# Performance work log

Measured on AMD Instinct MI355X. Metric: run time of the kernel, lower is better.

The kernel has to match this reference:

```python
import jax, jax.numpy as jnp
import numpy as np

D_FEATURE = 512
D_K = 512
B, LQ, N = 64, 128, 2048
NEG_BIAS = 1e10


def setup_inputs() -> dict:
    key = jax.random.key(0)
    k1, k2, k3, k4, k5, k6 = jax.random.split(key, 6)
    # xavier_uniform bound for Linear(d_feature -> d_k), weight shape [d_k, d_feature]
    bound = float(np.sqrt(6.0 / (D_FEATURE + D_K)))
    metal_feature = jax.random.normal(k1, (B, LQ, D_FEATURE), dtype=jnp.float32)
    x = jax.random.normal(k2, (B, N, D_FEATURE), dtype=jnp.float32)
    mask = jax.random.randint(k3, (B, N), 0, 2, dtype=jnp.int32)
    W_q = jax.random.uniform(k4, (D_K, D_FEATURE), jnp.float32, -bound, bound)
    W_k = jax.random.uniform(k5, (D_K, D_FEATURE), jnp.float32, -bound, bound)
    W_v = jax.random.uniform(k6, (D_K, D_FEATURE), jnp.float32, -bound, bound)
    return {"metal_feature": metal_feature, "x": x, "mask": mask,
            "W_q": W_q, "W_k": W_k, "W_v": W_v}


def reference(metal_feature, x, mask, W_q, W_k, W_v):
    # Q: [B, Lq, d_k], K/V: [B, N, d_k]  (torch Linear: y = x @ W.T, no bias)
    Q = jnp.einsum('blf,kf->blk', metal_feature, W_q)
    K = jnp.einsum('bnf,kf->bnk', x, W_k)
    V = jnp.einsum('bnf,kf->bnk', x, W_v)
    scale = 1.0 / jnp.sqrt(jnp.float32(D_K))
    # scores: [B, Lq, N] with additive mask bias (mask broadcast over queries)
    scores = jnp.einsum('blk,bnk->bln', Q, K) * scale
    scores = scores - (1.0 - mask[:, None, :].astype(scores.dtype)) * NEG_BIAS
    attn = jax.nn.softmax(scores, axis=-1)
    out = jnp.einsum('bln,bnk->blk', attn, V)
    # relu; squeeze(1) is a no-op for Lq>1; dropout identity at eval
    return jax.nn.relu(out)
```

## Files before the change

### kernel.cpp

```cpp
#include <hip/hip_runtime.h>

typedef __attribute__((ext_vector_type(4))) float   f32x4;
typedef __attribute__((ext_vector_type(8))) __bf16  bf16x8;
typedef unsigned short u16;
typedef __attribute__((ext_vector_type(8))) unsigned short u16x8;
typedef __attribute__((ext_vector_type(4))) unsigned short u16x4;

__device__ __forceinline__ u16 f2bf(float f) {
  unsigned u = __builtin_bit_cast(unsigned, f);
  u += 0x7fffu + ((u >> 16) & 1u);
  return (u16)(u >> 16);
}
__device__ __forceinline__ float bf2f(u16 h) {
  unsigned u = ((unsigned)h) << 16;
  return __builtin_bit_cast(float, u);
}
__device__ __forceinline__ void gld16(const void* g, void* l) {
  __builtin_amdgcn_global_load_lds(
      (const __attribute__((address_space(1))) void*)g,
      (__attribute__((address_space(3))) void*)l, 16, 0, 0);
}


#define SB __builtin_amdgcn_sched_barrier(0)
#define SYNC_MID do { SB; __builtin_amdgcn_s_barrier(); \
  asm volatile("s_waitcnt lgkmcnt(0)" ::: "memory"); SB; } while(0)
#define SYNC_END do { SB; __builtin_amdgcn_s_barrier(); SB; } while(0)
#define VM4 do { SB; asm volatile("s_waitcnt vmcnt(4)" ::: "memory"); SB; } while(0)
#define VM0 do { SB; asm volatile("s_waitcnt vmcnt(0)" ::: "memory"); SB; } while(0)

#define LDA(AQ, S, I0) \
  _Pragma("unroll") for (int f = 0; f < 2; ++f) \
  _Pragma("unroll") for (int s = 0; s < 2; ++s) { \
    const int rl = ((I0)+f)*16 + lr; \
    AQ[f*2+s] = *(const u16x8*)&SM[((S)*2 + wr)*8192 + rl*64 + (((s*4+lc) ^ (rl&7))*8)]; }

#define LDB(S) \
  _Pragma("unroll") for (int j = 0; j < 4; ++j) \
  _Pragma("unroll") for (int s = 0; s < 2; ++s) { \
    const int rl = (wc&1)*64 + j*16 + lr; \
    bq[j][s] = *(const u16x8*)&SM[32768 + ((S)*2 + (wc>>1))*8192 + rl*64 + (((s*4+lc) ^ (rl&7))*8)]; }

#define MM(AQ, I0) do { __builtin_amdgcn_s_setprio(1); \
  _Pragma("unroll") for (int f = 0; f < 2; ++f) \
  _Pragma("unroll") for (int j = 0; j < 4; ++j) \
  _Pragma("unroll") for (int s = 0; s < 2; ++s) \
    acc[(I0)+f][j] = __builtin_amdgcn_mfma_f32_16x16x32_bf16( \
      __builtin_bit_cast(bf16x8, AQ[f*2+s]), __builtin_bit_cast(bf16x8, bq[j][s]), \
      acc[(I0)+f][j], 0, 0, 0); \
  __builtin_amdgcn_s_setprio(0); } while(0)

__global__ __launch_bounds__(512, 1)
void kv8_k(const u16* __restrict__ xb, const u16* __restrict__ Wkv,
           u16* __restrict__ Kc, u16* __restrict__ Vt)
{
  __shared__ u16 SM[65536];
  const int t = threadIdx.x;
  const int w = t >> 6, lane = t & 63;
  const int wr = w >> 2, wc = w & 3;
  const int lr = lane & 15, lc = lane >> 4;

  int bx, by;
  if (gridDim.y == 64) {
    const int h = (int)(blockIdx.y * 4 + blockIdx.x);
    const int c = h & 7, i = h >> 3;
    by = c + 8 * (i & 7);
    bx = i >> 3;
  } else { bx = blockIdx.x; by = blockIdx.y; }
  const int n0 = bx * 256;
  const u16* xg = xb + (long)by * 2048 * 512;

  f32x4 acc[8][4];
#pragma unroll
  for (int i = 0; i < 8; i++)
#pragma unroll
    for (int j = 0; j < 4; j++) acc[i][j] = f32x4{0.f, 0.f, 0.f, 0.f};
  u16x8 bq[4][2];

  auto stageA = [&](int TT, int h) {
#pragma unroll
    for (int r = 0; r < 2; ++r) {
      const int c = r * 512 + t;
      const int row = c >> 3, slot = c & 7;
      const u16* g = xg + (long)((TT >> 3) * 256 + h * 128 + row) * 512
                        + (TT & 7) * 64 + ((slot ^ (row & 7)) * 8);
      gld16(g, (void*)&SM[((TT & 1) * 2 + h) * 8192 + c * 8]);
    }
  };
  auto stageB = [&](int TT, int h) {
#pragma unroll
    for (int r = 0; r < 2; ++r) {
      const int c = r * 512 + t;
      const int row = c >> 3, slot = c & 7;
      const u16* g = Wkv + (long)(n0 + h * 128 + row) * 512
                         + (TT & 7) * 64 + ((slot ^ (row & 7)) * 8);
      gld16(g, (void*)&SM[32768 + ((TT & 1) * 2 + h) * 8192 + c * 8]);
    }
  };
  auto epi = [&](int mt) {
#pragma unroll
    for (int i = 0; i < 8; i++)
#pragma unroll
      for (int j = 0; j < 4; j++) {
        const int ml = mt * 256 + wr * 128 + i * 16 + lc * 4;
        const int n  = n0 + wc * 64 + j * 16 + lr;
        if (n0 < 512) {
#pragma unroll
          for (int ii = 0; ii < 4; ii++)
            Kc[((long)by * 2048 + ml + ii) * 512 + n] = f2bf(acc[i][j][ii]);
        } else {
          u16x4 hh;
#pragma unroll
          for (int ii = 0; ii < 4; ii++) hh[ii] = f2bf(acc[i][j][ii]);
          *(u16x4*)(Vt + ((long)by * 512 + (n - 512)) * 2048 + ml) = hh;
        }
        acc[i][j] = f32x4{0.f, 0.f, 0.f, 0.f};
      }
  };

  stageA(0, 0); stageA(0, 1);
  stageB(0, 0); stageB(0, 1);
  stageB(1, 0); stageB(1, 1);
  VM4;
  __builtin_amdgcn_s_barrier(); SB;

  const int NT = 64;
#pragma unroll 1
  for (int I = 0; I < NT / 2; ++I) {
    const int a = 2 * I, b = 2 * I + 1;
    const bool g2 = (a + 2) < NT;
    const bool g3 = (b + 2) < NT;
    { u16x8 aq[4]; LDB(0); LDA(aq, 0, 0); stageA(b, 0);
      SYNC_MID; MM(aq, 0); SYNC_END; }
    { u16x8 aq[4]; LDA(aq, 0, 2); stageA(b, 1);
      SYNC_MID; MM(aq, 2); SYNC_END; }
    { u16x8 aq[4]; LDA(aq, 0, 4); if (g2) stageB(a + 2, 0);
      SYNC_MID; MM(aq, 4); SYNC_END; }
    { u16x8 aq[4]; LDA(aq, 0, 6); if (g2) stageB(a + 2, 1);
      SYNC_MID; MM(aq, 6); if (g2) { VM4; } else { VM0; } SYNC_END; }
    { u16x8 aq[4]; LDB(1); LDA(aq, 1, 0); if (g2) stageA(a + 2, 0);
      SYNC_MID; MM(aq, 0); SYNC_END; }
    { u16x8 aq[4]; LDA(aq, 1, 2); if (g2) stageA(a + 2, 1);
      SYNC_MID; MM(aq, 2); SYNC_END; }
    { u16x8 aq[4]; LDA(aq, 1, 4); if (g3) stageB(b + 2, 0);
      SYNC_MID; MM(aq, 4); SYNC_END; }
    { u16x8 aq[4]; LDA(aq, 1, 6); if (g3) stageB(b + 2, 1);
      SYNC_MID; MM(aq, 6); if (g3) { VM4; } else { VM0; } SYNC_END; }
    if ((I & 3) == 3) epi(I >> 2);
  }
}

template<int EPI>
__global__ __launch_bounds__(256)
void gemm_k(const u16* __restrict__ Ap, const u16* __restrict__ Bp,
            void* __restrict__ Cp, const int* __restrict__ maskp,
            int K, long sA, long sB, long sC, long sM, int ldc, float scale)
{
  __shared__ u16 Asb[2][4096];
  __shared__ u16 Bs [2][4096];

  const int t = threadIdx.x, z = blockIdx.z;
  const int n0 = blockIdx.x * 128, m0 = blockIdx.y * 128;
  const int KT = K / 32;
  const u16* Ab = Ap + (long)z * sA;
  const u16* Bb = Bp + (long)z * sB;

  const int w = t >> 6, lane = t & 63;
  const int m0w = (w >> 1) * 64, n0w = (w & 1) * 64;
  const int lr = lane & 15, lc = lane >> 4;

  f32x4 acc[4][4];
#pragma unroll
  for (int i = 0; i < 4; i++)
#pragma unroll
    for (int j = 0; j < 4; j++) acc[i][j] = f32x4{0.f, 0.f, 0.f, 0.f};

  auto stage = [&](int buf, int kt) {
#pragma unroll
    for (int i = 0; i < 2; i++) {
      int chunk = w * 2 + i, row = chunk * 16 + (lane >> 2), cc = lane & 3;
      const u16* g = Ab + (long)(m0 + row) * K + kt * 32 + ((cc ^ ((row >> 1) & 3)) << 3);
      gld16(g, (void*)&Asb[buf][chunk * 512]);
    }
#pragma unroll
    for (int i = 0; i < 2; i++) {
      int chunk = w * 2 + i, row = chunk * 16 + (lane >> 2), cc = lane & 3;
      const u16* g = Bb + (long)(n0 + row) * K + kt * 32 + ((cc ^ ((row >> 1) & 3)) << 3);
      gld16(g, (void*)&Bs[buf][chunk * 512]);
    }
  };
  auto compute = [&](int buf) {
    bf16x8 af[4], bv[4];
#pragma unroll
    for (int f = 0; f < 4; f++) {
      const int R = m0w + f * 16 + lr;
      af[f] = __builtin_bit_cast(bf16x8,
          *(const u16x8*)&Asb[buf][R * 32 + ((lc ^ ((R >> 1) & 3)) << 3)]);
      const int R2 = n0w + f * 16 + lr;
      bv[f] = __builtin_bit_cast(bf16x8,
          *(const u16x8*)&Bs[buf][R2 * 32 + ((lc ^ ((R2 >> 1) & 3)) << 3)]);
    }
#pragma unroll
    for (int i = 0; i < 4; i++)
#pragma unroll
      for (int j = 0; j < 4; j++)
        acc[i][j] = __builtin_amdgcn_mfma_f32_16x16x32_bf16(af[i], bv[j], acc[i][j], 0, 0, 0);
  };

  stage(0, 0);
  __syncthreads();
  int cur = 0;
  for (int kt = 1; kt < KT; ++kt) {
    stage(cur ^ 1, kt);
    compute(cur);
    __syncthreads();
    cur ^= 1;
  }
  compute(cur);

#pragma unroll
  for (int i = 0; i < 4; i++) {
#pragma unroll
    for (int j = 0; j < 4; j++) {
      const int mb = m0 + m0w + i * 16 + lc * 4;
      const int n  = n0 + n0w + j * 16 + lr;
      if constexpr (EPI == 0) {
        u16* C = (u16*)Cp + (long)z * sC;
#pragma unroll
        for (int ii = 0; ii < 4; ii++)
          C[(long)(mb + ii) * ldc + n] = f2bf(acc[i][j][ii]);
      } else if constexpr (EPI == 2) {
        const int* mk = maskp + (long)z * sM;
        u16* C = (u16*)Cp + (long)z * sC;
        const float bias = mk[n] ? 0.f : -1e10f;
#pragma unroll
        for (int ii = 0; ii < 4; ii++)
          C[(long)(mb + ii) * ldc + n] = f2bf(acc[i][j][ii] * scale + bias);
      } else {
        float* C = (float*)Cp + (long)z * sC;
#pragma unroll
        for (int ii = 0; ii < 4; ii++)
          C[(long)(mb + ii) * ldc + n] = fmaxf(acc[i][j][ii], 0.f);
      }
    }
  }
}

__global__ __launch_bounds__(256)
void wconv_k(const float* __restrict__ Wq, const float* __restrict__ Wk,
             const float* __restrict__ Wv, u16* __restrict__ Wb)
{
  long i4 = (long)blockIdx.x * 256 + threadIdx.x;
  long e  = i4 * 4;
  const float* W = (e < 262144) ? Wq : (e < 524288 ? Wk : Wv);
  long off = e & 262143;
  f32x4 f = *(const f32x4*)(W + off);
  u16x4 h;
#pragma unroll
  for (int j = 0; j < 4; j++) h[j] = f2bf(f[j]);
  *(u16x4*)(Wb + e) = h;
}

__global__ __launch_bounds__(256)
void cvt_k(const float* __restrict__ in, u16* __restrict__ out)
{
  long i = ((long)blockIdx.x * 256 + threadIdx.x) * 8;
  f32x4 a = *(const f32x4*)(in + i);
  f32x4 b = *(const f32x4*)(in + i + 4);
  u16x8 h;
#pragma unroll
  for (int j = 0; j < 4; j++) { h[j] = f2bf(a[j]); h[4 + j] = f2bf(b[j]); }
  *(u16x8*)(out + i) = h;
}

__global__ __launch_bounds__(256)
void softmax_k(u16* __restrict__ S)
{
  const long row = blockIdx.x;
  const int  t   = threadIdx.x;
  u16* R = S + row * 2048;
  u16x8 v = *(const u16x8*)(R + t * 8);
  float f[8];
#pragma unroll
  for (int j = 0; j < 8; j++) f[j] = bf2f(v[j]);
  float m = f[0];
#pragma unroll
  for (int j = 1; j < 8; j++) m = fmaxf(m, f[j]);
#pragma unroll
  for (int off = 32; off > 0; off >>= 1) m = fmaxf(m, __shfl_xor(m, off));
  __shared__ float red[4], red2[4];
  const int w = t >> 6;
  if ((t & 63) == 0) red[w] = m;
  __syncthreads();
  m = fmaxf(fmaxf(red[0], red[1]), fmaxf(red[2], red[3]));
  float e[8], s = 0.f;
#pragma unroll
  for (int j = 0; j < 8; j++) { e[j] = __expf(f[j] - m); s += e[j]; }
#pragma unroll
  for (int off = 32; off > 0; off >>= 1) s += __shfl_xor(s, off);
  if ((t & 63) == 0) red2[w] = s;
  __syncthreads();
  s = red2[0] + red2[1] + red2[2] + red2[3];
  const float inv = 1.f / s;
  u16x8 o;
#pragma unroll
  for (int j = 0; j < 8; j++) o[j] = f2bf(e[j] * inv);
  *(u16x8*)(R + t * 8) = o;
}

extern "C" void kernel_launch(void* const* d_in, const int* in_sizes, int n_in,
                              void* d_out, int out_size, void* d_ws, size_t ws_size,
                              hipStream_t stream)
{
  const float* mf   = (const float*)d_in[0];
  const float* x    = (const float*)d_in[1];
  const int*   mask = (const int*)d_in[2];
  const float* Wq   = (const float*)d_in[3];
  const float* Wk   = (const float*)d_in[4];
  const float* Wv   = (const float*)d_in[5];
  float* out = (float*)d_out;

  u16* ws  = (u16*)d_ws;
  u16* Wb  = ws;
  u16* mfb = Wb + 786432;
  u16* Qb  = mfb + 4194304;
  u16* dyn = Qb + 4194304;

  const size_t fixedB = (size_t)(786432 + 4194304 + 4194304) * 2;
  int CB = 64;
  while (CB > 1 && fixedB + (size_t)CB * 6815744ull > ws_size) CB >>= 1;

  u16* xbc = dyn;
  u16* Kc  = xbc + (size_t)CB * 1048576;
  u16* Vtc = Kc  + (size_t)CB * 1048576;
  u16* Sc  = Vtc + (size_t)CB * 1048576;

  const float scale = 0.044194173824159216f;

  wconv_k<<<768, 256, 0, stream>>>(Wq, Wk, Wv, Wb);
  cvt_k<<<2048, 256, 0, stream>>>(mf, mfb);

  gemm_k<0><<<dim3(4, 64, 1), 256, 0, stream>>>(
      mfb, Wb, Qb, nullptr, 512, 0, 0, 0, 0, 512, 1.f);

  for (int bc = 0; bc < 64; bc += CB) {
    const float* xc = x + (long)bc * 2048 * 512;
    cvt_k<<<CB * 512, 256, 0, stream>>>(xc, xbc);
    kv8_k<<<dim3(4, CB, 1), 512, 0, stream>>>(xbc, Wb + 262144, Kc, Vtc);
    gemm_k<2><<<dim3(16, 1, CB), 256, 0, stream>>>(
        Qb + (long)bc * 65536, Kc, Sc, mask + (long)bc * 2048,
        512, 65536, 1048576, 262144, 2048, 2048, scale);
    softmax_k<<<CB * 128, 256, 0, stream>>>(Sc);
    gemm_k<3><<<dim3(4, 1, CB), 256, 0, stream>>>(
        Sc, Vtc, out + (long)bc * 65536, nullptr,
        2048, 262144, 1048576, 65536, 0, 512, 1.f);
  }
}
```

Measured before the change: 392.0 us.

## Fuse fp32-to-bf16 conversion of x into KV GEMM via producer warps

Removes the separate cvt_k pass over x and its bf16 workspace buffer. The KV projection kernel gains 256 producer threads that load fp32 x tiles into registers, convert them to bf16 and write them into shared memory. They stay in lockstep with the 512 MFMA consumer threads through the existing barrier schedule. This saves a full read and write of x in bf16 and one kernel launch, at the cost of more threads and registers per block and a producer path that may not keep pace with the MFMA loop.

```diff
diff --git a/kernel.cpp b/kernel.cpp
--- a/kernel.cpp
+++ b/kernel.cpp
@@ -23,8 +23,8 @@
 
 
 #define SB __builtin_amdgcn_sched_barrier(0)
-#define SYNC_MID do { SB; __builtin_amdgcn_s_barrier(); \
-  asm volatile("s_waitcnt lgkmcnt(0)" ::: "memory"); SB; } while(0)
+#define LK0 asm volatile("s_waitcnt lgkmcnt(0)" ::: "memory")
+#define SYNC_MID do { SB; __builtin_amdgcn_s_barrier(); LK0; SB; } while(0)
 #define SYNC_END do { SB; __builtin_amdgcn_s_barrier(); SB; } while(0)
 #define VM4 do { SB; asm volatile("s_waitcnt vmcnt(4)" ::: "memory"); SB; } while(0)
 #define VM0 do { SB; asm volatile("s_waitcnt vmcnt(0)" ::: "memory"); SB; } while(0)
@@ -50,15 +50,12 @@
       acc[(I0)+f][j], 0, 0, 0); \
   __builtin_amdgcn_s_setprio(0); } while(0)
 
-__global__ __launch_bounds__(512, 1)
-void kv8_k(const u16* __restrict__ xb, const u16* __restrict__ Wkv,
+__global__ __launch_bounds__(768, 3)
+void kv8_k(const float* __restrict__ x, const u16* __restrict__ Wkv,
            u16* __restrict__ Kc, u16* __restrict__ Vt)
 {
   __shared__ u16 SM[65536];
   const int t = threadIdx.x;
-  const int w = t >> 6, lane = t & 63;
-  const int wr = w >> 2, wc = w & 3;
-  const int lr = lane & 15, lc = lane >> 4;
 
   int bx, by;
   if (gridDim.y == 64) {
@@ -68,85 +65,131 @@
     bx = i >> 3;
   } else { bx = blockIdx.x; by = blockIdx.y; }
   const int n0 = bx * 256;
-  const u16* xg = xb + (long)by * 2048 * 512;
-
-  f32x4 acc[8][4];
-#pragma unroll
-  for (int i = 0; i < 8; i++)
-#pragma unroll
-    for (int j = 0; j < 4; j++) acc[i][j] = f32x4{0.f, 0.f, 0.f, 0.f};
-  u16x8 bq[4][2];
-
-  auto stageA = [&](int TT, int h) {
-#pragma unroll
-    for (int r = 0; r < 2; ++r) {
-      const int c = r * 512 + t;
-      const int row = c >> 3, slot = c & 7;
-      const u16* g = xg + (long)((TT >> 3) * 256 + h * 128 + row) * 512
-                        + (TT & 7) * 64 + ((slot ^ (row & 7)) * 8);
-      gld16(g, (void*)&SM[((TT & 1) * 2 + h) * 8192 + c * 8]);
-    }
-  };
-  auto stageB = [&](int TT, int h) {
-#pragma unroll
-    for (int r = 0; r < 2; ++r) {
-      const int c = r * 512 + t;
-      const int row = c >> 3, slot = c & 7;
-      const u16* g = Wkv + (long)(n0 + h * 128 + row) * 512
-                         + (TT & 7) * 64 + ((slot ^ (row & 7)) * 8);
-      gld16(g, (void*)&SM[32768 + ((TT & 1) * 2 + h) * 8192 + c * 8]);
-    }
-  };
-  auto epi = [&](int mt) {
+  const float* xgf = x + (long)by * 2048 * 512;
+
+  const int NT = 64;
+
+  if (t < 512) {
+    const int w = t >> 6, lane = t & 63;
+    const int wr = w >> 2, wc = w & 3;
+    const int lr = lane & 15, lc = lane >> 4;
+
+    f32x4 acc[8][4];
 #pragma unroll
     for (int i = 0; i < 8; i++)
 #pragma unroll
-      for (int j = 0; j < 4; j++) {
-        const int ml = mt * 256 + wr * 128 + i * 16 + lc * 4;
-        const int n  = n0 + wc * 64 + j * 16 + lr;
-        if (n0 < 512) {
-#pragma unroll
-          for (int ii = 0; ii < 4; ii++)
-            Kc[((long)by * 2048 + ml + ii) * 512 + n] = f2bf(acc[i][j][ii]);
-        } else {
-          u16x4 hh;
-#pragma unroll
-          for (int ii = 0; ii < 4; ii++) hh[ii] = f2bf(acc[i][j][ii]);
-          *(u16x4*)(Vt + ((long)by * 512 + (n - 512)) * 2048 + ml) = hh;
+      for (int j = 0; j < 4; j++) acc[i][j] = f32x4{0.f, 0.f, 0.f, 0.f};
+    u16x8 bq[4][2];
+
+    auto stageB = [&](int TT, int h) {
+#pragma unroll
+      for (int r = 0; r < 2; ++r) {
+        const int c = r * 512 + t;
+        const int row = c >> 3, slot = c & 7;
+        const u16* g = Wkv + (long)(n0 + h * 128 + row) * 512
+                           + (TT & 7) * 64 + ((slot ^ (row & 7)) * 8);
+        gld16(g, (void*)&SM[32768 + ((TT & 1) * 2 + h) * 8192 + c * 8]);
+      }
+    };
+    auto epi = [&](int mt) {
+#pragma unroll
+      for (int i = 0; i < 8; i++)
+#pragma unroll
+        for (int j = 0; j < 4; j++) {
+          const int ml = mt * 256 + wr * 128 + i * 16 + lc * 4;
+          const int n  = n0 + wc * 64 + j * 16 + lr;
+          if (n0 < 512) {
+#pragma unroll
+            for (int ii = 0; ii < 4; ii++)
+              Kc[((long)by * 2048 + ml + ii) * 512 + n] = f2bf(acc[i][j][ii]);
+          } else {
+            u16x4 hh;
+#pragma unroll
+            for (int ii = 0; ii < 4; ii++) hh[ii] = f2bf(acc[i][j][ii]);
+            *(u16x4*)(Vt + ((long)by * 512 + (n - 512)) * 2048 + ml) = hh;
+          }
+          acc[i][j] = f32x4{0.f, 0.f, 0.f, 0.f};
         }
-        acc[i][j] = f32x4{0.f, 0.f, 0.f, 0.f};
+    };
+
+    stageB(0, 0); stageB(0, 1);
+    stageB(1, 0); stageB(1, 1);
+    VM4;
+    __builtin_amdgcn_s_barrier(); SB;
+
+#pragma unroll 1
+    for (int I = 0; I < NT / 2; ++I) {
+      const int a = 2 * I, b = 2 * I + 1;
+      const bool g2 = (a + 2) < NT;
+      const bool g3 = (b + 2) < NT;
+      { u16x8 aq[4]; LDB(0); LDA(aq, 0, 0);
+        SYNC_MID; MM(aq, 0); SYNC_END; }
+      { u16x8 aq[4]; LDA(aq, 0, 2);
+        SYNC_MID; MM(aq, 2); SYNC_END; }
+      { u16x8 aq[4]; LDA(aq, 0, 4); if (g2) stageB(a + 2, 0);
+        SYNC_MID; MM(aq, 4); SYNC_END; }
+      { u16x8 aq[4]; LDA(aq, 0, 6); if (g2) stageB(a + 2, 1);
+        SYNC_MID; MM(aq, 6); if (g2) { VM4; } else { VM0; } SYNC_END; }
+      { u16x8 aq[4]; LDB(1); LDA(aq, 1, 0);
+        SYNC_MID; MM(aq, 0); SYNC_END; }
+      { u16x8 aq[4]; LDA(aq, 1, 2);
+        SYNC_MID; MM(aq, 2); SYNC_END; }
+      { u16x8 aq[4]; LDA(aq, 1, 4); if (g3) stageB(b + 2, 0);
+        SYNC_MID; MM(aq, 4); SYNC_END; }
+      { u16x8 aq[4]; LDA(aq, 1, 6); if (g3) stageB(b + 2, 1);
+        SYNC_MID; MM(aq, 6); if (g3) { VM4; } else { VM0; } SYNC_END; }
+      if ((I & 3) == 3) epi(I >> 2);
+    }
+  } else {
+    const int pt = t - 512;
+
+    f32x4 P0[8], P1[8], P2[8], P3[8];
+
+    auto pissue = [&](f32x4* P, int TT, int h) {
+#pragma unroll
+      for (int r = 0; r < 4; ++r) {
+        const int c = r * 256 + pt;
+        const int row = c >> 3, slot = c & 7;
+        const float* g = xgf + (long)((TT >> 3) * 256 + h * 128 + row) * 512
+                             + (TT & 7) * 64 + ((slot ^ (row & 7)) * 8);
+        P[2 * r]     = *(const f32x4*)g;
+        P[2 * r + 1] = *(const f32x4*)(g + 4);
       }
-  };
-
-  stageA(0, 0); stageA(0, 1);
-  stageB(0, 0); stageB(0, 1);
-  stageB(1, 0); stageB(1, 1);
-  VM4;
-  __builtin_amdgcn_s_barrier(); SB;
-
-  const int NT = 64;
+    };
+    auto pwrite = [&](const f32x4* P, int TT, int h) {
+#pragma unroll
+      for (int r = 0; r < 4; ++r) {
+        const int c = r * 256 + pt;
+        u16x8 o;
+#pragma unroll
+        for (int j = 0; j < 4; ++j) {
+          o[j]     = f2bf(P[2 * r][j]);
+          o[4 + j] = f2bf(P[2 * r + 1][j]);
+        }
+        *(u16x8*)&SM[((TT & 1) * 2 + h) * 8192 + c * 8] = o;
+      }
+    };
+
+    pissue(P2, 0, 0); pissue(P3, 0, 1);
+    pwrite(P2, 0, 0); pwrite(P3, 0, 1);
+    pissue(P0, 1, 0); pissue(P1, 1, 1);
+    LK0; SB;
+    __builtin_amdgcn_s_barrier(); SB;
+
 #pragma unroll 1
-  for (int I = 0; I < NT / 2; ++I) {
-    const int a = 2 * I, b = 2 * I + 1;
-    const bool g2 = (a + 2) < NT;
-    const bool g3 = (b + 2) < NT;
-    { u16x8 aq[4]; LDB(0); LDA(aq, 0, 0); stageA(b, 0);
-      SYNC_MID; MM(aq, 0); SYNC_END; }
-    { u16x8 aq[4]; LDA(aq, 0, 2); stageA(b, 1);
-      SYNC_MID; MM(aq, 2); SYNC_END; }
-    { u16x8 aq[4]; LDA(aq, 0, 4); if (g2) stageB(a + 2, 0);
-      SYNC_MID; MM(aq, 4); SYNC_END; }
-    { u16x8 aq[4]; LDA(aq, 0, 6); if (g2) stageB(a + 2, 1);
-      SYNC_MID; MM(aq, 6); if (g2) { VM4; } else { VM0; } SYNC_END; }
-    { u16x8 aq[4]; LDB(1); LDA(aq, 1, 0); if (g2) stageA(a + 2, 0);
-      SYNC_MID; MM(aq, 0); SYNC_END; }
-    { u16x8 aq[4]; LDA(aq, 1, 2); if (g2) stageA(a + 2, 1);
-      SYNC_MID; MM(aq, 2); SYNC_END; }
-    { u16x8 aq[4]; LDA(aq, 1, 4); if (g3) stageB(b + 2, 0);
-      SYNC_MID; MM(aq, 4); SYNC_END; }
-    { u16x8 aq[4]; LDA(aq, 1, 6); if (g3) stageB(b + 2, 1);
-      SYNC_MID; MM(aq, 6); if (g3) { VM4; } else { VM0; } SYNC_END; }
-    if ((I & 3) == 3) epi(I >> 2);
+    for (int I = 0; I < NT / 2; ++I) {
+      const int a = 2 * I, b = 2 * I + 1;
+      const int aT = (a + 2 < NT) ? a + 2 : NT - 2;
+      const int bT = (b + 2 < NT) ? b + 2 : NT - 1;
+      { pissue(P2, aT, 0); pwrite(P0, b, 0); LK0; SYNC_MID; SYNC_END; }
+      { SYNC_MID; SYNC_END; }
+      { pissue(P3, aT, 1); pwrite(P1, b, 1); LK0; SYNC_MID; SYNC_END; }
+      { SYNC_MID; SYNC_END; }
+      { pissue(P0, bT, 0); pwrite(P2, aT, 0); LK0; SYNC_MID; SYNC_END; }
+      { SYNC_MID; SYNC_END; }
+      { pissue(P1, bT, 1); pwrite(P3, aT, 1); LK0; SYNC_MID; SYNC_END; }
+      { SYNC_MID; SYNC_END; }
+    }
   }
 }
 
@@ -328,11 +371,10 @@
 
   const size_t fixedB = (size_t)(786432 + 4194304 + 4194304) * 2;
   int CB = 64;
-  while (CB > 1 && fixedB + (size_t)CB * 6815744ull > ws_size) CB >>= 1;
-
-  u16* xbc = dyn;
-  u16* Kc  = xbc + (size_t)CB * 1048576;
-  u16* Vtc = Kc  + (size_t)CB * 1048576;
+  while (CB > 1 && fixedB + (size_t)CB * 4718592ull > ws_size) CB >>= 1;
+
+  u16* Kc  = dyn;
+  u16* Vtc = Kc + (size_t)CB * 1048576;
   u16* Sc  = Vtc + (size_t)CB * 1048576;
 
   const float scale = 0.044194173824159216f;
@@ -345,8 +387,7 @@
 
   for (int bc = 0; bc < 64; bc += CB) {
     const float* xc = x + (long)bc * 2048 * 512;
-    cvt_k<<<CB * 512, 256, 0, stream>>>(xc, xbc);
-    kv8_k<<<dim3(4, CB, 1), 512, 0, stream>>>(xbc, Wb + 262144, Kc, Vtc);
+    kv8_k<<<dim3(4, CB, 1), 768, 0, stream>>>(xc, Wb + 262144, Kc, Vtc);
     gemm_k<2><<<dim3(16, 1, CB), 256, 0, stream>>>(
         Qb + (long)bc * 65536, Kc, Sc, mask + (long)bc * 2048,
         512, 65536, 1048576, 262144, 2048, 2048, scale);
```

Result: slower. 812.0 us (+107.1%).

## Fuse x fp32-to-bf16 conversion into KV projection GEMM A-operand loads

Applied to the files above, without the earlier changes.

Drops the separate cvt_k pass over x. The KV GEMM kernel now reads fp32 x straight from global memory into registers and converts it to bf16 there. Only the weight tile stays staged in shared memory, which halves the LDS footprint and the workspace needed per batch chunk. The cost is that A loads are no longer prefetched or shared through LDS. Each wave column and each of the four N-blocks re-reads fp32 x, roughly doubling the bytes read per element, and global load latency is exposed inside each MFMA step.

```diff
diff --git a/kernel.cpp b/kernel.cpp
--- a/kernel.cpp
+++ b/kernel.cpp
@@ -23,23 +23,28 @@
 
 
 #define SB __builtin_amdgcn_sched_barrier(0)
-#define SYNC_MID do { SB; __builtin_amdgcn_s_barrier(); \
-  asm volatile("s_waitcnt lgkmcnt(0)" ::: "memory"); SB; } while(0)
+#define LK0 asm volatile("s_waitcnt lgkmcnt(0)" ::: "memory")
+#define SYNC_MID do { SB; __builtin_amdgcn_s_barrier(); LK0; SB; } while(0)
 #define SYNC_END do { SB; __builtin_amdgcn_s_barrier(); SB; } while(0)
 #define VM4 do { SB; asm volatile("s_waitcnt vmcnt(4)" ::: "memory"); SB; } while(0)
-#define VM0 do { SB; asm volatile("s_waitcnt vmcnt(0)" ::: "memory"); SB; } while(0)
-
-#define LDA(AQ, S, I0) \
+
+#define FLDA(AQ, TT, I0) \
   _Pragma("unroll") for (int f = 0; f < 2; ++f) \
   _Pragma("unroll") for (int s = 0; s < 2; ++s) { \
-    const int rl = ((I0)+f)*16 + lr; \
-    AQ[f*2+s] = *(const u16x8*)&SM[((S)*2 + wr)*8192 + rl*64 + (((s*4+lc) ^ (rl&7))*8)]; }
+    const int rg = (((TT) >> 3) * 256) + wr * 128 + ((I0) + f) * 16 + lr; \
+    const float* g = xgf + (long)rg * 512 + (((TT) & 7) * 64) + ((s * 4 + lc) * 8); \
+    const f32x4 lo = *(const f32x4*)g; \
+    const f32x4 hi = *(const f32x4*)(g + 4); \
+    bf16x8 v; \
+    _Pragma("unroll") for (int j = 0; j < 4; ++j) { \
+      v[j] = (__bf16)lo[j]; v[4 + j] = (__bf16)hi[j]; } \
+    AQ[f*2+s] = __builtin_bit_cast(u16x8, v); }
 
 #define LDB(S) \
   _Pragma("unroll") for (int j = 0; j < 4; ++j) \
   _Pragma("unroll") for (int s = 0; s < 2; ++s) { \
     const int rl = (wc&1)*64 + j*16 + lr; \
-    bq[j][s] = *(const u16x8*)&SM[32768 + ((S)*2 + (wc>>1))*8192 + rl*64 + (((s*4+lc) ^ (rl&7))*8)]; }
+    bq[j][s] = *(const u16x8*)&SM[((S)*2 + (wc>>1))*8192 + rl*64 + (((s*4+lc) ^ (rl&7))*8)]; }
 
 #define MM(AQ, I0) do { __builtin_amdgcn_s_setprio(1); \
   _Pragma("unroll") for (int f = 0; f < 2; ++f) \
@@ -51,10 +56,10 @@
   __builtin_amdgcn_s_setprio(0); } while(0)
 
 __global__ __launch_bounds__(512, 1)
-void kv8_k(const u16* __restrict__ xb, const u16* __restrict__ Wkv,
+void kv8_k(const float* __restrict__ x, const u16* __restrict__ Wkv,
            u16* __restrict__ Kc, u16* __restrict__ Vt)
 {
-  __shared__ u16 SM[65536];
+  __shared__ u16 SM[32768];
   const int t = threadIdx.x;
   const int w = t >> 6, lane = t & 63;
   const int wr = w >> 2, wc = w & 3;
@@ -68,7 +73,7 @@
     bx = i >> 3;
   } else { bx = blockIdx.x; by = blockIdx.y; }
   const int n0 = bx * 256;
-  const u16* xg = xb + (long)by * 2048 * 512;
+  const float* xgf = x + (long)by * 2048 * 512;
 
   f32x4 acc[8][4];
 #pragma unroll
@@ -77,16 +82,6 @@
     for (int j = 0; j < 4; j++) acc[i][j] = f32x4{0.f, 0.f, 0.f, 0.f};
   u16x8 bq[4][2];
 
-  auto stageA = [&](int TT, int h) {
-#pragma unroll
-    for (int r = 0; r < 2; ++r) {
-      const int c = r * 512 + t;
-      const int row = c >> 3, slot = c & 7;
-      const u16* g = xg + (long)((TT >> 3) * 256 + h * 128 + row) * 512
-                        + (TT & 7) * 64 + ((slot ^ (row & 7)) * 8);
-      gld16(g, (void*)&SM[((TT & 1) * 2 + h) * 8192 + c * 8]);
-    }
-  };
   auto stageB = [&](int TT, int h) {
 #pragma unroll
     for (int r = 0; r < 2; ++r) {
@@ -94,7 +89,7 @@
       const int row = c >> 3, slot = c & 7;
       const u16* g = Wkv + (long)(n0 + h * 128 + row) * 512
                          + (TT & 7) * 64 + ((slot ^ (row & 7)) * 8);
-      gld16(g, (void*)&SM[32768 + ((TT & 1) * 2 + h) * 8192 + c * 8]);
+      gld16(g, (void*)&SM[((TT & 1) * 2 + h) * 8192 + c * 8]);
     }
   };
   auto epi = [&](int mt) {
@@ -118,7 +113,6 @@
       }
   };
 
-  stageA(0, 0); stageA(0, 1);
   stageB(0, 0); stageB(0, 1);
   stageB(1, 0); stageB(1, 1);
   VM4;
@@ -130,22 +124,22 @@
     const int a = 2 * I, b = 2 * I + 1;
     const bool g2 = (a + 2) < NT;
     const bool g3 = (b + 2) < NT;
-    { u16x8 aq[4]; LDB(0); LDA(aq, 0, 0); stageA(b, 0);
+    { u16x8 aq[4]; FLDA(aq, a, 0); LDB(0);
       SYNC_MID; MM(aq, 0); SYNC_END; }
-    { u16x8 aq[4]; LDA(aq, 0, 2); stageA(b, 1);
+    { u16x8 aq[4]; FLDA(aq, a, 2);
       SYNC_MID; MM(aq, 2); SYNC_END; }
-    { u16x8 aq[4]; LDA(aq, 0, 4); if (g2) stageB(a + 2, 0);
+    { u16x8 aq[4]; FLDA(aq, a, 4); if (g2) stageB(a + 2, 0);
       SYNC_MID; MM(aq, 4); SYNC_END; }
-    { u16x8 aq[4]; LDA(aq, 0, 6); if (g2) stageB(a + 2, 1);
-      SYNC_MID; MM(aq, 6); if (g2) { VM4; } else { VM0; } SYNC_END; }
-    { u16x8 aq[4]; LDB(1); LDA(aq, 1, 0); if (g2) stageA(a + 2, 0);
+    { u16x8 aq[4]; FLDA(aq, a, 6); if (g2) stageB(a + 2, 1);
+      SYNC_MID; MM(aq, 6); SYNC_END; }
+    { u16x8 aq[4]; FLDA(aq, b, 0); LDB(1);
       SYNC_MID; MM(aq, 0); SYNC_END; }
-    { u16x8 aq[4]; LDA(aq, 1, 2); if (g2) stageA(a + 2, 1);
+    { u16x8 aq[4]; FLDA(aq, b, 2);
       SYNC_MID; MM(aq, 2); SYNC_END; }
-    { u16x8 aq[4]; LDA(aq, 1, 4); if (g3) stageB(b + 2, 0);
+    { u16x8 aq[4]; FLDA(aq, b, 4); if (g3) stageB(b + 2, 0);
       SYNC_MID; MM(aq, 4); SYNC_END; }
-    { u16x8 aq[4]; LDA(aq, 1, 6); if (g3) stageB(b + 2, 1);
-      SYNC_MID; MM(aq, 6); if (g3) { VM4; } else { VM0; } SYNC_END; }
+    { u16x8 aq[4]; FLDA(aq, b, 6); if (g3) stageB(b + 2, 1);
+      SYNC_MID; MM(aq, 6); SYNC_END; }
     if ((I & 3) == 3) epi(I >> 2);
   }
 }
@@ -328,11 +322,10 @@
 
   const size_t fixedB = (size_t)(786432 + 4194304 + 4194304) * 2;
   int CB = 64;
-  while (CB > 1 && fixedB + (size_t)CB * 6815744ull > ws_size) CB >>= 1;
-
-  u16* xbc = dyn;
-  u16* Kc  = xbc + (size_t)CB * 1048576;
-  u16* Vtc = Kc  + (size_t)CB * 1048576;
+  while (CB > 1 && fixedB + (size_t)CB * 4718592ull > ws_size) CB >>= 1;
+
+  u16* Kc  = dyn;
+  u16* Vtc = Kc + (size_t)CB * 1048576;
   u16* Sc  = Vtc + (size_t)CB * 1048576;
 
   const float scale = 0.044194173824159216f;
@@ -345,8 +338,7 @@
 
   for (int bc = 0; bc < 64; bc += CB) {
     const float* xc = x + (long)bc * 2048 * 512;
-    cvt_k<<<CB * 512, 256, 0, stream>>>(xc, xbc);
-    kv8_k<<<dim3(4, CB, 1), 512, 0, stream>>>(xbc, Wb + 262144, Kc, Vtc);
+    kv8_k<<<dim3(4, CB, 1), 512, 0, stream>>>(xc, Wb + 262144, Kc, Vtc);
     gemm_k<2><<<dim3(16, 1, CB), 256, 0, stream>>>(
         Qb + (long)bc * 65536, Kc, Sc, mask + (long)bc * 2048,
         512, 65536, 1048576, 262144, 2048, 2048, scale);
```

New measurement: 855.6 us. 118% more time.

## Shrink KV projection GEMM tile to 128x128 with 256-thread blocks, two per CU

Applied to the files above, without the earlier changes.

The fused K/V projection kernel moves from 256x256 tiles computed by 512 threads, one block per CU, to 128x128 tiles with 256 threads and two blocks per CU. Shared memory is halved and the pipeline becomes a simpler double buffer that waits for all outstanding loads (vmcnt 0) every other k-step. The grid doubles in x to cover the output. The aim is more blocks for occupancy and latency hiding, at the cost of less data reuse per tile and a shallower prefetch pipeline.

```diff
diff --git a/kernel.cpp b/kernel.cpp
--- a/kernel.cpp
+++ b/kernel.cpp
@@ -26,126 +26,119 @@
 #define SYNC_MID do { SB; __builtin_amdgcn_s_barrier(); \
   asm volatile("s_waitcnt lgkmcnt(0)" ::: "memory"); SB; } while(0)
 #define SYNC_END do { SB; __builtin_amdgcn_s_barrier(); SB; } while(0)
-#define VM4 do { SB; asm volatile("s_waitcnt vmcnt(4)" ::: "memory"); SB; } while(0)
 #define VM0 do { SB; asm volatile("s_waitcnt vmcnt(0)" ::: "memory"); SB; } while(0)
 
-#define LDA(AQ, S, I0) \
-  _Pragma("unroll") for (int f = 0; f < 2; ++f) \
-  _Pragma("unroll") for (int s = 0; s < 2; ++s) { \
-    const int rl = ((I0)+f)*16 + lr; \
-    AQ[f*2+s] = *(const u16x8*)&SM[((S)*2 + wr)*8192 + rl*64 + (((s*4+lc) ^ (rl&7))*8)]; }
-
-#define LDB(S) \
+#define LDA4(AQ, S, KS) \
+  _Pragma("unroll") for (int fi = 0; fi < 4; ++fi) { \
+    const int rl = wr * 64 + fi * 16 + lr; \
+    AQ[fi] = *(const u16x8*)&SM[(S) * 8192 + rl * 64 + ((((KS) * 4 + lc) ^ (rl & 7)) * 8)]; }
+
+#define LDB4(BQ, S, KS) \
+  _Pragma("unroll") for (int j = 0; j < 4; ++j) { \
+    const int rn = wc * 64 + j * 16 + lr; \
+    BQ[j] = *(const u16x8*)&SM[16384 + (S) * 8192 + rn * 64 + ((((KS) * 4 + lc) ^ (rn & 7)) * 8)]; }
+
+#define MM16(AQ, BQ) do { __builtin_amdgcn_s_setprio(1); \
+  _Pragma("unroll") for (int fi = 0; fi < 4; ++fi) \
   _Pragma("unroll") for (int j = 0; j < 4; ++j) \
-  _Pragma("unroll") for (int s = 0; s < 2; ++s) { \
-    const int rl = (wc&1)*64 + j*16 + lr; \
-    bq[j][s] = *(const u16x8*)&SM[32768 + ((S)*2 + (wc>>1))*8192 + rl*64 + (((s*4+lc) ^ (rl&7))*8)]; }
-
-#define MM(AQ, I0) do { __builtin_amdgcn_s_setprio(1); \
-  _Pragma("unroll") for (int f = 0; f < 2; ++f) \
-  _Pragma("unroll") for (int j = 0; j < 4; ++j) \
-  _Pragma("unroll") for (int s = 0; s < 2; ++s) \
-    acc[(I0)+f][j] = __builtin_amdgcn_mfma_f32_16x16x32_bf16( \
-      __builtin_bit_cast(bf16x8, AQ[f*2+s]), __builtin_bit_cast(bf16x8, bq[j][s]), \
-      acc[(I0)+f][j], 0, 0, 0); \
+    acc[fi][j] = __builtin_amdgcn_mfma_f32_16x16x32_bf16( \
+      __builtin_bit_cast(bf16x8, AQ[fi]), __builtin_bit_cast(bf16x8, BQ[j]), \
+      acc[fi][j], 0, 0, 0); \
   __builtin_amdgcn_s_setprio(0); } while(0)
 
-__global__ __launch_bounds__(512, 1)
+__global__ __launch_bounds__(256, 2)
 void kv8_k(const u16* __restrict__ xb, const u16* __restrict__ Wkv,
            u16* __restrict__ Kc, u16* __restrict__ Vt)
 {
-  __shared__ u16 SM[65536];
+  __shared__ u16 SM[32768];
   const int t = threadIdx.x;
   const int w = t >> 6, lane = t & 63;
-  const int wr = w >> 2, wc = w & 3;
+  const int wr = w >> 1, wc = w & 1;
   const int lr = lane & 15, lc = lane >> 4;
 
   int bx, by;
-  if (gridDim.y == 64) {
-    const int h = (int)(blockIdx.y * 4 + blockIdx.x);
+  if (gridDim.y == 64 && gridDim.x == 8) {
+    const int h = (int)(blockIdx.y * 8 + blockIdx.x);
     const int c = h & 7, i = h >> 3;
     by = c + 8 * (i & 7);
     bx = i >> 3;
   } else { bx = blockIdx.x; by = blockIdx.y; }
-  const int n0 = bx * 256;
+  const int n0 = bx * 128;
   const u16* xg = xb + (long)by * 2048 * 512;
 
-  f32x4 acc[8][4];
-#pragma unroll
-  for (int i = 0; i < 8; i++)
+  f32x4 acc[4][4];
+#pragma unroll
+  for (int i = 0; i < 4; i++)
 #pragma unroll
     for (int j = 0; j < 4; j++) acc[i][j] = f32x4{0.f, 0.f, 0.f, 0.f};
-  u16x8 bq[4][2];
 
   auto stageA = [&](int TT, int h) {
 #pragma unroll
     for (int r = 0; r < 2; ++r) {
-      const int c = r * 512 + t;
-      const int row = c >> 3, slot = c & 7;
-      const u16* g = xg + (long)((TT >> 3) * 256 + h * 128 + row) * 512
-                        + (TT & 7) * 64 + ((slot ^ (row & 7)) * 8);
-      gld16(g, (void*)&SM[((TT & 1) * 2 + h) * 8192 + c * 8]);
+      const int c = r * 256 + t;
+      const int row64 = c >> 3, sl = c & 7;
+      const int row = h * 64 + row64;
+      const u16* g = xg + (long)((TT >> 3) * 128 + row) * 512
+                        + (TT & 7) * 64 + ((sl ^ (row & 7)) * 8);
+      gld16(g, (void*)&SM[(TT & 1) * 8192 + h * 4096 + c * 8]);
     }
   };
   auto stageB = [&](int TT, int h) {
 #pragma unroll
     for (int r = 0; r < 2; ++r) {
-      const int c = r * 512 + t;
-      const int row = c >> 3, slot = c & 7;
-      const u16* g = Wkv + (long)(n0 + h * 128 + row) * 512
-                         + (TT & 7) * 64 + ((slot ^ (row & 7)) * 8);
-      gld16(g, (void*)&SM[32768 + ((TT & 1) * 2 + h) * 8192 + c * 8]);
+      const int c = r * 256 + t;
+      const int row64 = c >> 3, sl = c & 7;
+      const int row = h * 64 + row64;
+      const u16* g = Wkv + (long)(n0 + row) * 512
+                         + (TT & 7) * 64 + ((sl ^ (row & 7)) * 8);
+      gld16(g, (void*)&SM[16384 + (TT & 1) * 8192 + h * 4096 + c * 8]);
     }
   };
   auto epi = [&](int mt) {
 #pragma unroll
-    for (int i = 0; i < 8; i++)
+    for (int fi = 0; fi < 4; fi++)
 #pragma unroll
       for (int j = 0; j < 4; j++) {
-        const int ml = mt * 256 + wr * 128 + i * 16 + lc * 4;
+        const int ml = mt * 128 + wr * 64 + fi * 16 + lc * 4;
         const int n  = n0 + wc * 64 + j * 16 + lr;
         if (n0 < 512) {
 #pragma unroll
           for (int ii = 0; ii < 4; ii++)
-            Kc[((long)by * 2048 + ml + ii) * 512 + n] = f2bf(acc[i][j][ii]);
+            Kc[((long)by * 2048 + ml + ii) * 512 + n] = f2bf(acc[fi][j][ii]);
         } else {
           u16x4 hh;
 #pragma unroll
-          for (int ii = 0; ii < 4; ii++) hh[ii] = f2bf(acc[i][j][ii]);
+          for (int ii = 0; ii < 4; ii++) hh[ii] = f2bf(acc[fi][j][ii]);
           *(u16x4*)(Vt + ((long)by * 512 + (n - 512)) * 2048 + ml) = hh;
         }
-        acc[i][j] = f32x4{0.f, 0.f, 0.f, 0.f};
+        acc[fi][j] = f32x4{0.f, 0.f, 0.f, 0.f};
       }
   };
 
   stageA(0, 0); stageA(0, 1);
   stageB(0, 0); stageB(0, 1);
-  stageB(1, 0); stageB(1, 1);
-  VM4;
+  VM0;
   __builtin_amdgcn_s_barrier(); SB;
 
-  const int NT = 64;
+  const int NT = 128;
 #pragma unroll 1
   for (int I = 0; I < NT / 2; ++I) {
     const int a = 2 * I, b = 2 * I + 1;
     const bool g2 = (a + 2) < NT;
-    const bool g3 = (b + 2) < NT;
-    { u16x8 aq[4]; LDB(0); LDA(aq, 0, 0); stageA(b, 0);
-      SYNC_MID; MM(aq, 0); SYNC_END; }
-    { u16x8 aq[4]; LDA(aq, 0, 2); stageA(b, 1);
-      SYNC_MID; MM(aq, 2); SYNC_END; }
-    { u16x8 aq[4]; LDA(aq, 0, 4); if (g2) stageB(a + 2, 0);
-      SYNC_MID; MM(aq, 4); SYNC_END; }
-    { u16x8 aq[4]; LDA(aq, 0, 6); if (g2) stageB(a + 2, 1);
-      SYNC_MID; MM(aq, 6); if (g2) { VM4; } else { VM0; } SYNC_END; }
-    { u16x8 aq[4]; LDB(1); LDA(aq, 1, 0); if (g2) stageA(a + 2, 0);
-      SYNC_MID; MM(aq, 0); SYNC_END; }
-    { u16x8 aq[4]; LDA(aq, 1, 2); if (g2) stageA(a + 2, 1);
-      SYNC_MID; MM(aq, 2); SYNC_END; }
-    { u16x8 aq[4]; LDA(aq, 1, 4); if (g3) stageB(b + 2, 0);
-      SYNC_MID; MM(aq, 4); SYNC_END; }
-    { u16x8 aq[4]; LDA(aq, 1, 6); if (g3) stageB(b + 2, 1);
-      SYNC_MID; MM(aq, 6); if (g3) { VM4; } else { VM0; } SYNC_END; }
+    { u16x8 aq[4], bq[4];
+      LDA4(aq, 0, 0); LDB4(bq, 0, 0);
+      stageA(b, 0); stageA(b, 1); stageB(b, 0); stageB(b, 1);
+      SYNC_MID; MM16(aq, bq); SYNC_END; }
+    { u16x8 aq[4], bq[4];
+      LDA4(aq, 0, 1); LDB4(bq, 0, 1);
+      SYNC_MID; MM16(aq, bq); VM0; SYNC_END; }
+    { u16x8 aq[4], bq[4];
+      LDA4(aq, 1, 0); LDB4(bq, 1, 0);
+      if (g2) { stageA(a + 2, 0); stageA(a + 2, 1); stageB(a + 2, 0); stageB(a + 2, 1); }
+      SYNC_MID; MM16(aq, bq); SYNC_END; }
+    { u16x8 aq[4], bq[4];
+      LDA4(aq, 1, 1); LDB4(bq, 1, 1);
+      SYNC_MID; MM16(aq, bq); VM0; SYNC_END; }
     if ((I & 3) == 3) epi(I >> 2);
   }
 }
@@ -346,7 +339,7 @@
   for (int bc = 0; bc < 64; bc += CB) {
     const float* xc = x + (long)bc * 2048 * 512;
     cvt_k<<<CB * 512, 256, 0, stream>>>(xc, xbc);
-    kv8_k<<<dim3(4, CB, 1), 512, 0, stream>>>(xbc, Wb + 262144, Kc, Vtc);
+    kv8_k<<<dim3(8, CB, 1), 256, 0, stream>>>(xbc, Wb + 262144, Kc, Vtc);
     gemm_k<2><<<dim3(16, 1, CB), 256, 0, stream>>>(
         Qb + (long)bc * 65536, Kc, Sc, mask + (long)bc * 2048,
         512, 65536, 1048576, 262144, 2048, 2048, scale);
```

New measurement: 424.6 us. 8.3% more time.
